# Kernel optimization log

Hardware: AMD Instinct MI355X
Metric: run time of the kernel (lower is better)

Reference implementation:

```python
import jax, jax.numpy as jnp
import numpy as np

U = 8          # units per modular layer
B = 16384      # batch
IN = 512       # input feature dim
H = 512        # modular hidden dim
NC = 62        # n_class


def _aggregate(P, h):
    # P: [T, F] policy link matrix; h: [F, B, D] per-unit features.
    # agg[t] = sum_f P[t,f] * h[f], normalized by row-sum when row-sum > 0.
    s = jnp.einsum('tf,fbd->tbd', P, h)
    row = P.sum(axis=1)                      # [T]
    safe = jnp.where(row > 0, row, 1.0)[:, None, None]
    return jnp.where((row > 0)[:, None, None], s / safe, s)


def setup_inputs() -> dict:
    key = jax.random.key(0)
    ks = jax.random.split(key, 12)
    s_in = 1.0 / np.sqrt(IN)
    s_h = 1.0 / np.sqrt(H)
    return {
        'x': jax.random.normal(ks[0], (B, IN), jnp.float32),
        'policy1': jax.random.uniform(ks[1], (U * U,), jnp.float32),
        'policy2': jax.random.uniform(ks[2], (U * U,), jnp.float32),
        'policy_final': jax.random.uniform(ks[3], (U,), jnp.float32),
        'W0': jax.random.uniform(ks[4], (U, IN, H), jnp.float32, -s_in, s_in),
        'b0': jax.random.uniform(ks[5], (U, H), jnp.float32, -s_in, s_in),
        'W1': jax.random.uniform(ks[6], (U, H, H), jnp.float32, -s_h, s_h),
        'b1': jax.random.uniform(ks[7], (U, H), jnp.float32, -s_h, s_h),
        'W2': jax.random.uniform(ks[8], (U, H, NC), jnp.float32, -s_h, s_h),
        'b2': jax.random.uniform(ks[9], (U, NC), jnp.float32, -s_h, s_h),
    }


def reference(x, policy1, policy2, policy_final, W0, b0, W1, b1, W2, b2):
    # Layer 0 (input modular layer): policy_list[0] is forced to all-ones,
    # so every unit sees x unscaled. Each unit: Linear + ReLU.
    h0 = jax.nn.relu(jnp.einsum('bi,uid->ubd', x, W0) + b0[:, None, :])  # [U,B,H]

    # Mid layer: policy-gated weighted-sum aggregation, then per-unit Linear+ReLU.
    a1 = _aggregate(policy1.reshape(U, U), h0)
    h1 = jax.nn.relu(jnp.einsum('ubi,uid->ubd', a1, W1) + b1[:, None, :])

    # Output modular layer: aggregate then per-unit Linear (no activation).
    a2 = _aggregate(policy2.reshape(U, U), h1)
    h2 = jnp.einsum('ubi,uic->ubc', a2, W2) + b2[:, None, :]  # [U,B,NC]

    # Final gating. Original code divides by divider INSIDE the unit loop
    # (every iteration), so replicate that recurrence exactly.
    d = policy_final.sum()
    inv = jnp.where(d > 0, 1.0 / jnp.where(d > 0, d, 1.0), 1.0)
    out = jnp.zeros((B, NC), jnp.float32)
    for j in range(U):  # fixed small unit count, not a data dim
        out = (out + h2[j] * policy_final[j]) * inv
    return out
```

## Files before the change

kernel.cpp:

```cpp
#include <hip/hip_runtime.h>

#define U_   8
#define B_   16384
#define NC_  62

typedef __attribute__((ext_vector_type(8))) short bfrag;
typedef __attribute__((ext_vector_type(4))) float facc;

__device__ __forceinline__ float bf2f(unsigned int lo16) {
    union { unsigned int i; float f; } v;
    v.i = lo16 << 16;
    return v.f;
}
__device__ __forceinline__ unsigned short f2bf(float f) {
    unsigned int x = __float_as_uint(f);
    return (unsigned short)((x + 0x7fffu + ((x >> 16) & 1u)) >> 16);
}
__device__ __forceinline__ void gl2lds16(const void* g, void* l) {
    __builtin_amdgcn_global_load_lds(
        (const __attribute__((address_space(1))) void*)g,
        (__attribute__((address_space(3))) void*)l, 16, 0, 0);
}
__device__ __forceinline__ void cfence() { asm volatile("" ::: "memory"); }
__device__ __forceinline__ void bar() {
    asm volatile("" ::: "memory");
    __builtin_amdgcn_s_barrier();
    asm volatile("" ::: "memory");
}
#define VMCNT(n) asm volatile("s_waitcnt vmcnt(" #n ")" ::: "memory")

__global__ void prep_kernel(const float* __restrict__ p1, const float* __restrict__ p2,
                            const float* __restrict__ pf, const float* __restrict__ b2,
                            float* __restrict__ P1n, float* __restrict__ P2n,
                            float* __restrict__ wfin, float* __restrict__ cconst)
{
    int t = threadIdx.x;
    if (t >= 64) return;
    int row = t >> 3;
    float s1 = 0.f, s2 = 0.f;
    for (int f = 0; f < 8; f++) { s1 += p1[row * 8 + f]; s2 += p2[row * 8 + f]; }
    P1n[t] = p1[t] * (s1 > 0.f ? 1.f / s1 : 1.f);
    P2n[t] = p2[t] * (s2 > 0.f ? 1.f / s2 : 1.f);
    float d = 0.f;
    for (int j = 0; j < 8; j++) d += pf[j];
    float inv = d > 0.f ? 1.f / d : 1.f;
    float wv[8];
    for (int j = 0; j < 8; j++) {
        float v = pf[j];
        for (int i = j; i < 8; i++) v *= inv;
        wv[j] = v;
    }
    if (t < 8) wfin[t] = wv[t];
    float cc = 0.f;
    if (t < NC_) for (int u = 0; u < 8; u++) cc += wv[u] * b2[u * NC_ + t];
    cconst[t] = cc;
}

__global__ __launch_bounds__(256) void reorder_w0(
    const float* __restrict__ W0, unsigned short* __restrict__ W0r)
{
    __shared__ float tile[32][33];
    const int u  = blockIdx.z;
    const int n0 = blockIdx.x * 32, k0 = blockIdx.y * 32;
    const int tx = threadIdx.x & 31, ty = threadIdx.x >> 5;
    const float* Wb = W0 + (long)u * 512 * 512;
#pragma unroll
    for (int i = 0; i < 4; i++)
        tile[ty + i * 8][tx] = Wb[(long)(k0 + ty + i * 8) * 512 + n0 + tx];
    __syncthreads();
#pragma unroll
    for (int i = 0; i < 4; i++) {
        int n = n0 + ty + i * 8, k = k0 + tx;
        int np = (n >> 5) * 256 + u * 32 + (n & 31);
        W0r[(long)np * 512 + k] = f2bf(tile[tx][ty + i * 8]);
    }
}

__global__ __launch_bounds__(256) void transpose_w(
    const float* __restrict__ W, unsigned short* __restrict__ Wt)
{
    __shared__ float tile[32][33];
    const int u  = blockIdx.z;
    const int n0 = blockIdx.x * 32, k0 = blockIdx.y * 32;
    const int tx = threadIdx.x & 31, ty = threadIdx.x >> 5;
    const float* Wb = W + (long)u * 512 * 512;
#pragma unroll
    for (int i = 0; i < 4; i++)
        tile[ty + i * 8][tx] = Wb[(long)(k0 + ty + i * 8) * 512 + n0 + tx];
    __syncthreads();
    unsigned short* Wo = Wt + (long)u * 512 * 512;
#pragma unroll
    for (int i = 0; i < 4; i++) {
        int n = n0 + ty + i * 8, k = k0 + tx;
        Wo[(long)n * 512 + k] = f2bf(tile[tx][ty + i * 8]);
    }
}

__global__ __launch_bounds__(256) void wout_build(
    const float* __restrict__ W2, const float* __restrict__ P2n,
    const float* __restrict__ wfin, unsigned short* __restrict__ Woutt)
{
    const int c   = threadIdx.x & 63;
    const int row = blockIdx.x * 4 + (threadIdx.x >> 6);
    const int f = row >> 9, k = row & 511;
    float s = 0.f;
    if (c < NC_) {
#pragma unroll
        for (int u = 0; u < 8; u++)
            s += wfin[u] * P2n[u * 8 + f] * W2[((long)u * 512 + k) * NC_ + c];
    }
    Woutt[(long)c * 4096 + row] = f2bf(s);
}

__global__ __launch_bounds__(256) void convert_x(
    const float* __restrict__ x, unsigned short* __restrict__ xb, long n)
{
    long i = ((long)blockIdx.x * 256 + threadIdx.x) * 8;
    if (i >= n) return;
    const float4* xp = (const float4*)(x + i);
    float4 a = xp[0], b = xp[1];
    uint4 o;
    o.x = f2bf(a.x) | ((unsigned)f2bf(a.y) << 16);
    o.y = f2bf(a.z) | ((unsigned)f2bf(a.w) << 16);
    o.z = f2bf(b.x) | ((unsigned)f2bf(b.y) << 16);
    o.w = f2bf(b.z) | ((unsigned)f2bf(b.w) << 16);
    *(uint4*)(xb + i) = o;
}

__global__ __launch_bounds__(512, 2) void gemm0_mix(
    const unsigned short* __restrict__ xb, const unsigned short* __restrict__ W0r,
    const float* __restrict__ b0, const float* __restrict__ P1n,
    unsigned short* __restrict__ a1, long plane)
{
    __shared__ __align__(16) unsigned short sm[49152];
    const int tid = threadIdx.x, w = tid >> 6, lane = tid & 63;
    const int flat = blockIdx.x;
    const int xcd = flat & 7, seq = flat >> 3;
    const int ng = xcd * 2 + (seq & 1);
    const long mBase = (long)(seq >> 1) * 128;

    const int lr = lane >> 3;
    const int lg = (lane & 7) ^ lr;
    const int wm = w >> 2, wn = w & 3;
    const int r = lane & 15, q = lane >> 4;
    const int x7 = r & 7;

    facc acc[4][4];
#pragma unroll
    for (int i = 0; i < 4; i++)
#pragma unroll
        for (int j = 0; j < 4; j++) acc[i][j] = (facc){0.f, 0.f, 0.f, 0.f};

    auto stage = [&](int buf, int kt) {
        const int k0 = kt * 64;
        unsigned short* dA = sm + buf * 8192;
        unsigned short* dB = sm + 16384 + buf * 16384;
#pragma unroll
        for (int i = 0; i < 2; i++) {
            const int c = w + i * 8;
            gl2lds16(xb + (mBase + c * 8 + lr) * 512 + k0 + lg * 8, dA + c * 512);
        }
#pragma unroll
        for (int i = 0; i < 4; i++) {
            const int c = w * 4 + i;
            gl2lds16(W0r + ((long)ng * 256 + c * 8 + lr) * 512 + k0 + lg * 8,
                     dB + c * 512);
        }
    };
    auto compute = [&](int buf) {
        const unsigned short* sA = sm + buf * 8192;
        const unsigned short* sB = sm + 16384 + buf * 16384;
#pragma unroll
        for (int h = 0; h < 2; h++) {
            const int xg = ((h * 4 + q) ^ x7) * 8;
            bfrag aF[4], bF[4];
#pragma unroll
            for (int mt = 0; mt < 4; mt++)
                aF[mt] = *(const bfrag*)&sA[(wm * 64 + mt * 16 + r) * 64 + xg];
#pragma unroll
            for (int nt = 0; nt < 4; nt++)
                bF[nt] = *(const bfrag*)&sB[(wn * 64 + nt * 16 + r) * 64 + xg];
#pragma unroll
            for (int mt = 0; mt < 4; mt++)
#pragma unroll
                for (int nt = 0; nt < 4; nt++)
                    acc[mt][nt] = __builtin_amdgcn_mfma_f32_16x16x32_bf16(
                        aF[mt], bF[nt], acc[mt][nt], 0, 0, 0);
        }
    };

    stage(0, 0);
    cfence();
    stage(1, 1);
    VMCNT(6);
    bar();
#pragma unroll
    for (int t = 0; t < 8; ++t) {
        compute(t & 1);
        if (t <= 5) {
            bar();
            stage(t & 1, t + 2);
            VMCNT(6);
            bar();
        } else if (t == 6) {
            VMCNT(0);
            bar();
        } else {
            bar();
        }
    }

#pragma unroll
    for (int nt = 0; nt < 4; nt++) {
        const int cl = wn * 64 + nt * 16 + r;
        const float bv = b0[(cl >> 5) * 512 + ng * 32 + (cl & 31)];
#pragma unroll
        for (int mt = 0; mt < 4; mt++) {
            const int rowb = wm * 64 + mt * 16 + q * 4;
#pragma unroll
            for (int rg = 0; rg < 4; rg++) {
                float v = acc[mt][nt][rg] + bv;
                v = v > 0.f ? v : 0.f;
                sm[(rowb + rg) * 264 + cl] = f2bf(v);
            }
        }
    }
    __syncthreads();

    float pw[64];
#pragma unroll
    for (int i = 0; i < 64; i++) pw[i] = P1n[i];
    const int row = tid >> 2, fs = (tid & 3) * 8;
    float hv[8][8];
#pragma unroll
    for (int u = 0; u < 8; u++) {
        bfrag hx = *(const bfrag*)&sm[row * 264 + u * 32 + fs];
#pragma unroll
        for (int j = 0; j < 8; j++)
            hv[u][j] = bf2f((unsigned int)(unsigned short)hx[j]);
    }
    const long rowOff = (mBase + row) * 512 + ng * 32 + fs;
#pragma unroll
    for (int t = 0; t < 8; t++) {
        float o[8];
#pragma unroll
        for (int j = 0; j < 8; j++) {
            float s = 0.f;
#pragma unroll
            for (int u = 0; u < 8; u++) s = fmaf(pw[t * 8 + u], hv[u][j], s);
            o[j] = s;
        }
        uint4 ov;
        ov.x = f2bf(o[0]) | ((unsigned)f2bf(o[1]) << 16);
        ov.y = f2bf(o[2]) | ((unsigned)f2bf(o[3]) << 16);
        ov.z = f2bf(o[4]) | ((unsigned)f2bf(o[5]) << 16);
        ov.w = f2bf(o[6]) | ((unsigned)f2bf(o[7]) << 16);
        *(uint4*)(a1 + (long)t * plane + rowOff) = ov;
    }
}

__global__ __launch_bounds__(256, 2) void gemm_h(
    const unsigned short* __restrict__ a1,
    const unsigned short* __restrict__ W1t,
    const float* __restrict__ b1,
    unsigned short* __restrict__ h1, long plane)
{
    __shared__ __align__(16) unsigned short sm[32768];
    const int tid = threadIdx.x, w = tid >> 6, lane = tid & 63;
    const int flat = blockIdx.x;
    const int u = flat & 7, seq = flat >> 3;
    const int nBase = (seq & 3) * 128;
    const long mBase = (long)(seq >> 2) * 128;

    const int lr = lane >> 3, lg = (lane & 7) ^ lr;
    const int wm = w >> 1, wn = w & 1;
    const int r = lane & 15, q = lane >> 4;
    const int x7 = r & 7;

    const unsigned short* Ab = a1 + (long)u * plane;
    const unsigned short* Bb = W1t + ((long)u * 512 + nBase) * 512;

    facc acc[4][4];
#pragma unroll
    for (int i = 0; i < 4; i++)
#pragma unroll
        for (int j = 0; j < 4; j++) acc[i][j] = (facc){0.f, 0.f, 0.f, 0.f};

    auto stage = [&](int buf, int kt) {
        const int k0 = kt * 64;
        unsigned short* dA = sm + buf * 8192;
        unsigned short* dB = sm + 16384 + buf * 8192;
#pragma unroll
        for (int i = 0; i < 4; i++) {
            const int c = w * 4 + i;
            gl2lds16(Ab + (mBase + c * 8 + lr) * 512 + k0 + lg * 8, dA + c * 512);
            gl2lds16(Bb + (long)(c * 8 + lr) * 512 + k0 + lg * 8, dB + c * 512);
        }
    };
    auto compute = [&](int buf) {
        const unsigned short* sA = sm + buf * 8192;
        const unsigned short* sB = sm + 16384 + buf * 8192;
#pragma unroll
        for (int h = 0; h < 2; h++) {
            const int xg = ((h * 4 + q) ^ x7) * 8;
            bfrag aF[4], bF[4];
#pragma unroll
            for (int mt = 0; mt < 4; mt++)
                aF[mt] = *(const bfrag*)&sA[(wm * 64 + mt * 16 + r) * 64 + xg];
#pragma unroll
            for (int nt = 0; nt < 4; nt++)
                bF[nt] = *(const bfrag*)&sB[(wn * 64 + nt * 16 + r) * 64 + xg];
#pragma unroll
            for (int mt = 0; mt < 4; mt++)
#pragma unroll
                for (int nt = 0; nt < 4; nt++)
                    acc[mt][nt] = __builtin_amdgcn_mfma_f32_16x16x32_bf16(
                        aF[mt], bF[nt], acc[mt][nt], 0, 0, 0);
        }
    };

    stage(0, 0);
    cfence();
    stage(1, 1);
    VMCNT(8);
    bar();
#pragma unroll
    for (int t = 0; t < 8; ++t) {
        compute(t & 1);
        if (t <= 5) {
            bar();
            stage(t & 1, t + 2);
            VMCNT(8);
            bar();
        } else if (t == 6) {
            VMCNT(0);
            bar();
        } else {
            bar();
        }
    }

#pragma unroll
    for (int nt = 0; nt < 4; nt++) {
        const int col = wn * 64 + nt * 16 + r;
        const float bv = b1[u * 512 + nBase + col];
#pragma unroll
        for (int mt = 0; mt < 4; mt++) {
            const int rowb = wm * 64 + mt * 16 + q * 4;
#pragma unroll
            for (int rg = 0; rg < 4; rg++) {
                float v = acc[mt][nt][rg] + bv;
                v = v > 0.f ? v : 0.f;
                sm[(rowb + rg) * 136 + col] = f2bf(v);
            }
        }
    }
    __syncthreads();

    unsigned short* Cb = h1 + (long)u * plane + mBase * 512 + nBase;
#pragma unroll
    for (int it = 0; it < 8; it++) {
        const int g = tid + it * 256;
        const int row = g >> 4, gr = g & 15;
        *(uint4*)(Cb + (long)row * 512 + gr * 8) = *(const uint4*)&sm[row * 136 + gr * 8];
    }
}

__global__ __launch_bounds__(256, 1) void gemm_out(
    const unsigned short* __restrict__ h1,
    const unsigned short* __restrict__ Bt,
    float* __restrict__ partial, long plane, int Bc)
{
    __shared__ __align__(16) unsigned short sm[16384];
    const int tid = threadIdx.x, w = tid >> 6, lane = tid & 63;
    const int flat = blockIdx.x;
    const int kc = flat & 1;
    const long mBase = (long)(flat >> 1) * 64;

    const int lr = lane >> 3, lg = (lane & 7) ^ lr;
    const int wm = w >> 1, wn = w & 1;
    const int r = lane & 15, q = lane >> 4;
    const int x7 = r & 7;

    facc acc[2][2];
#pragma unroll
    for (int i = 0; i < 2; i++)
#pragma unroll
        for (int j = 0; j < 2; j++) acc[i][j] = (facc){0.f, 0.f, 0.f, 0.f};

    auto stage = [&](int buf, int it) {
        const int u = kc * 4 + (it >> 3);
        const int kk = (it & 7) * 64;
        unsigned short* dA = sm + buf * 4096;
        unsigned short* dB = sm + 8192 + buf * 4096;
#pragma unroll
        for (int i = 0; i < 2; i++) {
            const int c = w * 2 + i;
            gl2lds16(h1 + (long)u * plane + (mBase + c * 8 + lr) * 512 + kk + lg * 8,
                     dA + c * 512);
            gl2lds16(Bt + (long)(c * 8 + lr) * 4096 + u * 512 + kk + lg * 8,
                     dB + c * 512);
        }
    };
    auto compute = [&](int buf) {
        const unsigned short* sA = sm + buf * 4096;
        const unsigned short* sB = sm + 8192 + buf * 4096;
#pragma unroll
        for (int h = 0; h < 2; h++) {
            const int xg = ((h * 4 + q) ^ x7) * 8;
            bfrag aF[2], bF[2];
#pragma unroll
            for (int mt = 0; mt < 2; mt++)
                aF[mt] = *(const bfrag*)&sA[(wm * 32 + mt * 16 + r) * 64 + xg];
#pragma unroll
            for (int nt = 0; nt < 2; nt++)
                bF[nt] = *(const bfrag*)&sB[(wn * 32 + nt * 16 + r) * 64 + xg];
#pragma unroll
            for (int mt = 0; mt < 2; mt++)
#pragma unroll
                for (int nt = 0; nt < 2; nt++)
                    acc[mt][nt] = __builtin_amdgcn_mfma_f32_16x16x32_bf16(
                        aF[mt], bF[nt], acc[mt][nt], 0, 0, 0);
        }
    };

    stage(0, 0);
    cfence();
    stage(1, 1);
    VMCNT(4);
    bar();
#pragma unroll
    for (int t = 0; t < 32; ++t) {
        compute(t & 1);
        if (t <= 29) {
            bar();
            stage(t & 1, t + 2);
            VMCNT(4);
            bar();
        } else if (t == 30) {
            VMCNT(0);
            bar();
        }
    }

    float* pb = partial + ((long)kc * Bc + mBase) * 64;
#pragma unroll
    for (int nt = 0; nt < 2; nt++) {
        const int col = wn * 32 + nt * 16 + r;
#pragma unroll
        for (int mt = 0; mt < 2; mt++) {
#pragma unroll
            for (int rg = 0; rg < 4; rg++) {
                const int row = wm * 32 + mt * 16 + q * 4 + rg;
                pb[(long)row * 64 + col] = acc[mt][nt][rg];
            }
        }
    }
}

__global__ __launch_bounds__(256) void reduce_out(
    const float* __restrict__ partial, const float* __restrict__ cconst,
    float* __restrict__ out, int Bc)
{
    const long flat = (long)blockIdx.x * 256 + threadIdx.x;
    const long row = flat >> 2;
    const int cg = (int)(flat & 3) * 16;
    float s[16];
#pragma unroll
    for (int j = 0; j < 16; j++) s[j] = 0.f;
#pragma unroll
    for (int kc = 0; kc < 2; kc++) {
        const float4* p = (const float4*)(partial + ((long)kc * Bc + row) * 64 + cg);
#pragma unroll
        for (int v4 = 0; v4 < 4; v4++) {
            float4 v = p[v4];
            s[v4 * 4 + 0] += v.x; s[v4 * 4 + 1] += v.y;
            s[v4 * 4 + 2] += v.z; s[v4 * 4 + 3] += v.w;
        }
    }
#pragma unroll
    for (int j = 0; j < 16; j++) {
        const int c = cg + j;
        if (c < NC_) out[row * NC_ + c] = s[j] + cconst[c];
    }
}

extern "C" void kernel_launch(void* const* d_in, const int* in_sizes, int n_in,
                              void* d_out, int out_size, void* d_ws, size_t ws_size,
                              hipStream_t stream)
{
    const float* x  = (const float*)d_in[0];
    const float* p1 = (const float*)d_in[1];
    const float* p2 = (const float*)d_in[2];
    const float* pf = (const float*)d_in[3];
    const float* W0 = (const float*)d_in[4];
    const float* b0 = (const float*)d_in[5];
    const float* W1 = (const float*)d_in[6];
    const float* b1 = (const float*)d_in[7];
    const float* W2 = (const float*)d_in[8];
    const float* b2 = (const float*)d_in[9];
    float* out = (float*)d_out;

    char* ws = (char*)d_ws;
    size_t off = 0;
    auto alloc = [&](size_t bytes) -> void* {
        void* p = ws + off;
        off += (bytes + 255) & ~(size_t)255;
        return p;
    };
    float* P1n    = (float*)alloc(64 * sizeof(float));
    float* P2n    = (float*)alloc(64 * sizeof(float));
    float* wfin   = (float*)alloc(8 * sizeof(float));
    float* cconst = (float*)alloc(64 * sizeof(float));
    unsigned short* W0r   = (unsigned short*)alloc((size_t)4096 * 512 * 2);
    unsigned short* W1t   = (unsigned short*)alloc((size_t)U_ * 512 * 512 * 2);
    unsigned short* Woutt = (unsigned short*)alloc((size_t)64 * 4096 * 2);
    unsigned short* xb    = (unsigned short*)alloc((size_t)B_ * 512 * 2);

    size_t remain = ws_size > off ? ws_size - off : 0;
    int Bc = 2048;
    for (int cand = B_; cand >= 2048; cand >>= 1) {
        size_t need = 2ull * 8 * cand * 512 * 2 + 2ull * cand * 64 * 4 + 1024;
        if (need <= remain) { Bc = cand; break; }
    }
    unsigned short* a1 = (unsigned short*)alloc(8ull * Bc * 512 * 2);
    unsigned short* h1 = (unsigned short*)alloc(8ull * Bc * 512 * 2);
    float* partial     = (float*)alloc(2ull * Bc * 64 * 4);

    prep_kernel<<<1, 64, 0, stream>>>(p1, p2, pf, b2, P1n, P2n, wfin, cconst);
    reorder_w0<<<dim3(16, 16, 8), 256, 0, stream>>>(W0, W0r);
    transpose_w<<<dim3(16, 16, 8), 256, 0, stream>>>(W1, W1t);
    wout_build<<<dim3(1024), 256, 0, stream>>>(W2, P2n, wfin, Woutt);
    convert_x<<<dim3(B_ * 512 / 8 / 256), 256, 0, stream>>>(x, xb, (long)B_ * 512);

    const int Mb = Bc / 128;
    const long plane = (long)Bc * 512;
    for (int bb = 0; bb < B_; bb += Bc) {
        gemm0_mix<<<dim3(16 * Mb), 512, 0, stream>>>(
            xb + (long)bb * 512, W0r, b0, P1n, a1, plane);
        gemm_h<<<dim3(32 * Mb), 256, 0, stream>>>(a1, W1t, b1, h1, plane);
        gemm_out<<<dim3(2 * (Bc / 64)), 256, 0, stream>>>(h1, Woutt, partial, plane, Bc);
        reduce_out<<<dim3(Bc / 64), 256, 0, stream>>>(
            partial, cconst, out + (long)bb * NC_, Bc);
    }
}
```

Measured before the change: 315.6 us.

## Triple-buffer GEMM pipelines, widen gemm_h tile, add MFMA priority hints

The three GEMM kernels go from double to triple buffering in LDS. The next stage's loads are now issued before the current compute, which removes one barrier per iteration. gemm_h moves to 512-thread blocks with 128x256 tiles to match gemm0_mix and get more reuse of A, and MFMA blocks are wrapped in s_setprio to favour math issue. The cost is more LDS per block (144KB for gemm0/gemm_h at 2 blocks per CU), which may limit occupancy, and fewer blocks for gemm_h.

```diff
diff --git a/kernel.cpp b/kernel.cpp
--- a/kernel.cpp
+++ b/kernel.cpp
@@ -132,7 +132,7 @@
     const float* __restrict__ b0, const float* __restrict__ P1n,
     unsigned short* __restrict__ a1, long plane)
 {
-    __shared__ __align__(16) unsigned short sm[49152];
+    __shared__ __align__(16) unsigned short sm[73728];
     const int tid = threadIdx.x, w = tid >> 6, lane = tid & 63;
     const int flat = blockIdx.x;
     const int xcd = flat & 7, seq = flat >> 3;
@@ -154,7 +154,7 @@
     auto stage = [&](int buf, int kt) {
         const int k0 = kt * 64;
         unsigned short* dA = sm + buf * 8192;
-        unsigned short* dB = sm + 16384 + buf * 16384;
+        unsigned short* dB = sm + 24576 + buf * 16384;
 #pragma unroll
         for (int i = 0; i < 2; i++) {
             const int c = w + i * 8;
@@ -169,7 +169,7 @@
     };
     auto compute = [&](int buf) {
         const unsigned short* sA = sm + buf * 8192;
-        const unsigned short* sB = sm + 16384 + buf * 16384;
+        const unsigned short* sB = sm + 24576 + buf * 16384;
 #pragma unroll
         for (int h = 0; h < 2; h++) {
             const int xg = ((h * 4 + q) ^ x7) * 8;
@@ -180,12 +180,14 @@
 #pragma unroll
             for (int nt = 0; nt < 4; nt++)
                 bF[nt] = *(const bfrag*)&sB[(wn * 64 + nt * 16 + r) * 64 + xg];
+            __builtin_amdgcn_s_setprio(1);
 #pragma unroll
             for (int mt = 0; mt < 4; mt++)
 #pragma unroll
                 for (int nt = 0; nt < 4; nt++)
                     acc[mt][nt] = __builtin_amdgcn_mfma_f32_16x16x32_bf16(
                         aF[mt], bF[nt], acc[mt][nt], 0, 0, 0);
+            __builtin_amdgcn_s_setprio(0);
         }
     };
 
@@ -196,18 +198,11 @@
     bar();
 #pragma unroll
     for (int t = 0; t < 8; ++t) {
-        compute(t & 1);
-        if (t <= 5) {
-            bar();
-            stage(t & 1, t + 2);
-            VMCNT(6);
-            bar();
-        } else if (t == 6) {
-            VMCNT(0);
-            bar();
-        } else {
-            bar();
-        }
+        if (t < 6) stage((t + 2) % 3, t + 2);
+        compute(t % 3);
+        if (t < 6)       { VMCNT(6); bar(); }
+        else if (t == 6) { VMCNT(0); bar(); }
+        else             { bar(); }
     }
 
 #pragma unroll
@@ -259,129 +254,128 @@
     }
 }
 
-__global__ __launch_bounds__(256, 2) void gemm_h(
+__global__ __launch_bounds__(512, 2) void gemm_h(
     const unsigned short* __restrict__ a1,
     const unsigned short* __restrict__ W1t,
     const float* __restrict__ b1,
     unsigned short* __restrict__ h1, long plane)
 {
-    __shared__ __align__(16) unsigned short sm[32768];
+    __shared__ __align__(16) unsigned short sm[73728];
     const int tid = threadIdx.x, w = tid >> 6, lane = tid & 63;
     const int flat = blockIdx.x;
     const int u = flat & 7, seq = flat >> 3;
-    const int nBase = (seq & 3) * 128;
-    const long mBase = (long)(seq >> 2) * 128;
+    const int nBase = (seq & 1) * 256;
+    const long mBase = (long)(seq >> 1) * 128;
+
+    const int lr = lane >> 3, lg = (lane & 7) ^ lr;
+    const int wm = w >> 2, wn = w & 3;
+    const int r = lane & 15, q = lane >> 4;
+    const int x7 = r & 7;
+
+    const unsigned short* Ab = a1 + (long)u * plane;
+    const unsigned short* Bb = W1t + ((long)u * 512 + nBase) * 512;
+
+    facc acc[4][4];
+#pragma unroll
+    for (int i = 0; i < 4; i++)
+#pragma unroll
+        for (int j = 0; j < 4; j++) acc[i][j] = (facc){0.f, 0.f, 0.f, 0.f};
+
+    auto stage = [&](int buf, int kt) {
+        const int k0 = kt * 64;
+        unsigned short* dA = sm + buf * 8192;
+        unsigned short* dB = sm + 24576 + buf * 16384;
+#pragma unroll
+        for (int i = 0; i < 2; i++) {
+            const int c = w + i * 8;
+            gl2lds16(Ab + (mBase + c * 8 + lr) * 512 + k0 + lg * 8, dA + c * 512);
+        }
+#pragma unroll
+        for (int i = 0; i < 4; i++) {
+            const int c = w * 4 + i;
+            gl2lds16(Bb + (long)(c * 8 + lr) * 512 + k0 + lg * 8, dB + c * 512);
+        }
+    };
+    auto compute = [&](int buf) {
+        const unsigned short* sA = sm + buf * 8192;
+        const unsigned short* sB = sm + 24576 + buf * 16384;
+#pragma unroll
+        for (int h = 0; h < 2; h++) {
+            const int xg = ((h * 4 + q) ^ x7) * 8;
+            bfrag aF[4], bF[4];
+#pragma unroll
+            for (int mt = 0; mt < 4; mt++)
+                aF[mt] = *(const bfrag*)&sA[(wm * 64 + mt * 16 + r) * 64 + xg];
+#pragma unroll
+            for (int nt = 0; nt < 4; nt++)
+                bF[nt] = *(const bfrag*)&sB[(wn * 64 + nt * 16 + r) * 64 + xg];
+            __builtin_amdgcn_s_setprio(1);
+#pragma unroll
+            for (int mt = 0; mt < 4; mt++)
+#pragma unroll
+                for (int nt = 0; nt < 4; nt++)
+                    acc[mt][nt] = __builtin_amdgcn_mfma_f32_16x16x32_bf16(
+                        aF[mt], bF[nt], acc[mt][nt], 0, 0, 0);
+            __builtin_amdgcn_s_setprio(0);
+        }
+    };
+
+    stage(0, 0);
+    cfence();
+    stage(1, 1);
+    VMCNT(6);
+    bar();
+#pragma unroll
+    for (int t = 0; t < 8; ++t) {
+        if (t < 6) stage((t + 2) % 3, t + 2);
+        compute(t % 3);
+        if (t < 6)       { VMCNT(6); bar(); }
+        else if (t == 6) { VMCNT(0); bar(); }
+        else             { bar(); }
+    }
+
+#pragma unroll
+    for (int nt = 0; nt < 4; nt++) {
+        const int cl = wn * 64 + nt * 16 + r;
+        const float bv = b1[u * 512 + nBase + cl];
+#pragma unroll
+        for (int mt = 0; mt < 4; mt++) {
+            const int rowb = wm * 64 + mt * 16 + q * 4;
+#pragma unroll
+            for (int rg = 0; rg < 4; rg++) {
+                float v = acc[mt][nt][rg] + bv;
+                v = v > 0.f ? v : 0.f;
+                sm[(rowb + rg) * 264 + cl] = f2bf(v);
+            }
+        }
+    }
+    __syncthreads();
+
+    unsigned short* Cb = h1 + (long)u * plane + mBase * 512 + nBase;
+#pragma unroll
+    for (int it = 0; it < 8; it++) {
+        const int g = tid + it * 512;
+        const int row = g >> 5, gr = g & 31;
+        *(uint4*)(Cb + (long)row * 512 + gr * 8) = *(const uint4*)&sm[row * 264 + gr * 8];
+    }
+}
+
+__global__ __launch_bounds__(256, 1) void gemm_out(
+    const unsigned short* __restrict__ h1,
+    const unsigned short* __restrict__ Bt,
+    float* __restrict__ partial, long plane, int Bc)
+{
+    __shared__ __align__(16) unsigned short sm[24576];
+    const int tid = threadIdx.x, w = tid >> 6, lane = tid & 63;
+    const int flat = blockIdx.x;
+    const int kc = flat & 1;
+    const long mBase = (long)(flat >> 1) * 64;
 
     const int lr = lane >> 3, lg = (lane & 7) ^ lr;
     const int wm = w >> 1, wn = w & 1;
     const int r = lane & 15, q = lane >> 4;
     const int x7 = r & 7;
 
-    const unsigned short* Ab = a1 + (long)u * plane;
-    const unsigned short* Bb = W1t + ((long)u * 512 + nBase) * 512;
-
-    facc acc[4][4];
-#pragma unroll
-    for (int i = 0; i < 4; i++)
-#pragma unroll
-        for (int j = 0; j < 4; j++) acc[i][j] = (facc){0.f, 0.f, 0.f, 0.f};
-
-    auto stage = [&](int buf, int kt) {
-        const int k0 = kt * 64;
-        unsigned short* dA = sm + buf * 8192;
-        unsigned short* dB = sm + 16384 + buf * 8192;
-#pragma unroll
-        for (int i = 0; i < 4; i++) {
-            const int c = w * 4 + i;
-            gl2lds16(Ab + (mBase + c * 8 + lr) * 512 + k0 + lg * 8, dA + c * 512);
-            gl2lds16(Bb + (long)(c * 8 + lr) * 512 + k0 + lg * 8, dB + c * 512);
-        }
-    };
-    auto compute = [&](int buf) {
-        const unsigned short* sA = sm + buf * 8192;
-        const unsigned short* sB = sm + 16384 + buf * 8192;
-#pragma unroll
-        for (int h = 0; h < 2; h++) {
-            const int xg = ((h * 4 + q) ^ x7) * 8;
-            bfrag aF[4], bF[4];
-#pragma unroll
-            for (int mt = 0; mt < 4; mt++)
-                aF[mt] = *(const bfrag*)&sA[(wm * 64 + mt * 16 + r) * 64 + xg];
-#pragma unroll
-            for (int nt = 0; nt < 4; nt++)
-                bF[nt] = *(const bfrag*)&sB[(wn * 64 + nt * 16 + r) * 64 + xg];
-#pragma unroll
-            for (int mt = 0; mt < 4; mt++)
-#pragma unroll
-                for (int nt = 0; nt < 4; nt++)
-                    acc[mt][nt] = __builtin_amdgcn_mfma_f32_16x16x32_bf16(
-                        aF[mt], bF[nt], acc[mt][nt], 0, 0, 0);
-        }
-    };
-
-    stage(0, 0);
-    cfence();
-    stage(1, 1);
-    VMCNT(8);
-    bar();
-#pragma unroll
-    for (int t = 0; t < 8; ++t) {
-        compute(t & 1);
-        if (t <= 5) {
-            bar();
-            stage(t & 1, t + 2);
-            VMCNT(8);
-            bar();
-        } else if (t == 6) {
-            VMCNT(0);
-            bar();
-        } else {
-            bar();
-        }
-    }
-
-#pragma unroll
-    for (int nt = 0; nt < 4; nt++) {
-        const int col = wn * 64 + nt * 16 + r;
-        const float bv = b1[u * 512 + nBase + col];
-#pragma unroll
-        for (int mt = 0; mt < 4; mt++) {
-            const int rowb = wm * 64 + mt * 16 + q * 4;
-#pragma unroll
-            for (int rg = 0; rg < 4; rg++) {
-                float v = acc[mt][nt][rg] + bv;
-                v = v > 0.f ? v : 0.f;
-                sm[(rowb + rg) * 136 + col] = f2bf(v);
-            }
-        }
-    }
-    __syncthreads();
-
-    unsigned short* Cb = h1 + (long)u * plane + mBase * 512 + nBase;
-#pragma unroll
-    for (int it = 0; it < 8; it++) {
-        const int g = tid + it * 256;
-        const int row = g >> 4, gr = g & 15;
-        *(uint4*)(Cb + (long)row * 512 + gr * 8) = *(const uint4*)&sm[row * 136 + gr * 8];
-    }
-}
-
-__global__ __launch_bounds__(256, 1) void gemm_out(
-    const unsigned short* __restrict__ h1,
-    const unsigned short* __restrict__ Bt,
-    float* __restrict__ partial, long plane, int Bc)
-{
-    __shared__ __align__(16) unsigned short sm[16384];
-    const int tid = threadIdx.x, w = tid >> 6, lane = tid & 63;
-    const int flat = blockIdx.x;
-    const int kc = flat & 1;
-    const long mBase = (long)(flat >> 1) * 64;
-
-    const int lr = lane >> 3, lg = (lane & 7) ^ lr;
-    const int wm = w >> 1, wn = w & 1;
-    const int r = lane & 15, q = lane >> 4;
-    const int x7 = r & 7;
-
     facc acc[2][2];
 #pragma unroll
     for (int i = 0; i < 2; i++)
@@ -392,7 +386,7 @@
         const int u = kc * 4 + (it >> 3);
         const int kk = (it & 7) * 64;
         unsigned short* dA = sm + buf * 4096;
-        unsigned short* dB = sm + 8192 + buf * 4096;
+        unsigned short* dB = sm + 12288 + buf * 4096;
 #pragma unroll
         for (int i = 0; i < 2; i++) {
             const int c = w * 2 + i;
@@ -404,7 +398,7 @@
     };
     auto compute = [&](int buf) {
         const unsigned short* sA = sm + buf * 4096;
-        const unsigned short* sB = sm + 8192 + buf * 4096;
+        const unsigned short* sB = sm + 12288 + buf * 4096;
 #pragma unroll
         for (int h = 0; h < 2; h++) {
             const int xg = ((h * 4 + q) ^ x7) * 8;
@@ -415,12 +409,14 @@
 #pragma unroll
             for (int nt = 0; nt < 2; nt++)
                 bF[nt] = *(const bfrag*)&sB[(wn * 32 + nt * 16 + r) * 64 + xg];
+            __builtin_amdgcn_s_setprio(1);
 #pragma unroll
             for (int mt = 0; mt < 2; mt++)
 #pragma unroll
                 for (int nt = 0; nt < 2; nt++)
                     acc[mt][nt] = __builtin_amdgcn_mfma_f32_16x16x32_bf16(
                         aF[mt], bF[nt], acc[mt][nt], 0, 0, 0);
+            __builtin_amdgcn_s_setprio(0);
         }
     };
 
@@ -431,16 +427,10 @@
     bar();
 #pragma unroll
     for (int t = 0; t < 32; ++t) {
-        compute(t & 1);
-        if (t <= 29) {
-            bar();
-            stage(t & 1, t + 2);
-            VMCNT(4);
-            bar();
-        } else if (t == 30) {
-            VMCNT(0);
-            bar();
-        }
+        if (t < 30) stage((t + 2) % 3, t + 2);
+        compute(t % 3);
+        if (t < 30)       { VMCNT(4); bar(); }
+        else if (t == 30) { VMCNT(0); bar(); }
     }
 
     float* pb = partial + ((long)kc * Bc + mBase) * 64;
@@ -538,7 +528,7 @@
     for (int bb = 0; bb < B_; bb += Bc) {
         gemm0_mix<<<dim3(16 * Mb), 512, 0, stream>>>(
             xb + (long)bb * 512, W0r, b0, P1n, a1, plane);
-        gemm_h<<<dim3(32 * Mb), 256, 0, stream>>>(a1, W1t, b1, h1, plane);
+        gemm_h<<<dim3(16 * Mb), 512, 0, stream>>>(a1, W1t, b1, h1, plane);
         gemm_out<<<dim3(2 * (Bc / 64)), 256, 0, stream>>>(h1, Woutt, partial, plane, Bc);
         reduce_out<<<dim3(Bc / 64), 256, 0, stream>>>(
             partial, cconst, out + (long)bb * NC_, Bc);
```

Measured after the change: 338.4 us. 7.2% more time.

## Retile GEMMs to 128x256 per 4-wave block with BK=32 and LDS-wait barriers

Applied to the files above, without the earlier changes.

gemm0_mix moves from 512 threads with 4x4 tiles per wave to 256 threads with 4x8 tiles per wave. gemm_h widens its block N tile from 128 to 256, which halves its grid. Both kernels shrink the K step from 64 to 32 with a new XOR swizzle and double the iteration count. Barriers after compute now wait on lgkmcnt(0) before reusing the buffer. The larger per-wave tiles raise MFMA work per LDS fragment load and cut the shared-memory footprint, at the cost of higher accumulator register pressure and more barrier round-trips per K.

```diff
diff --git a/kernel.cpp b/kernel.cpp
--- a/kernel.cpp
+++ b/kernel.cpp
@@ -24,6 +24,11 @@
 __device__ __forceinline__ void cfence() { asm volatile("" ::: "memory"); }
 __device__ __forceinline__ void bar() {
     asm volatile("" ::: "memory");
+    __builtin_amdgcn_s_barrier();
+    asm volatile("" ::: "memory");
+}
+__device__ __forceinline__ void barL() {
+    asm volatile("s_waitcnt lgkmcnt(0)" ::: "memory");
     __builtin_amdgcn_s_barrier();
     asm volatile("" ::: "memory");
 }
@@ -127,66 +132,62 @@
     *(uint4*)(xb + i) = o;
 }
 
-__global__ __launch_bounds__(512, 2) void gemm0_mix(
+__global__ __launch_bounds__(256, 2) void gemm0_mix(
     const unsigned short* __restrict__ xb, const unsigned short* __restrict__ W0r,
     const float* __restrict__ b0, const float* __restrict__ P1n,
     unsigned short* __restrict__ a1, long plane)
 {
-    __shared__ __align__(16) unsigned short sm[49152];
+    __shared__ __align__(16) unsigned short sm[33792];
     const int tid = threadIdx.x, w = tid >> 6, lane = tid & 63;
     const int flat = blockIdx.x;
     const int xcd = flat & 7, seq = flat >> 3;
     const int ng = xcd * 2 + (seq & 1);
     const long mBase = (long)(seq >> 1) * 128;
 
-    const int lr = lane >> 3;
-    const int lg = (lane & 7) ^ lr;
-    const int wm = w >> 2, wn = w & 3;
+    const int lr = lane >> 2;
+    const int lg = (lane & 3) ^ ((lane >> 3) & 3);
+    const int wm = w >> 1, wn = w & 1;
     const int r = lane & 15, q = lane >> 4;
-    const int x7 = r & 7;
-
-    facc acc[4][4];
+    const int xq = (q ^ ((r >> 1) & 3)) * 8;
+
+    facc acc[4][8];
 #pragma unroll
     for (int i = 0; i < 4; i++)
 #pragma unroll
-        for (int j = 0; j < 4; j++) acc[i][j] = (facc){0.f, 0.f, 0.f, 0.f};
+        for (int j = 0; j < 8; j++) acc[i][j] = (facc){0.f, 0.f, 0.f, 0.f};
 
     auto stage = [&](int buf, int kt) {
-        const int k0 = kt * 64;
-        unsigned short* dA = sm + buf * 8192;
-        unsigned short* dB = sm + 16384 + buf * 16384;
+        const int k0 = kt * 32;
+        unsigned short* dA = sm + buf * 4096;
+        unsigned short* dB = sm + 8192 + buf * 8192;
 #pragma unroll
         for (int i = 0; i < 2; i++) {
-            const int c = w + i * 8;
-            gl2lds16(xb + (mBase + c * 8 + lr) * 512 + k0 + lg * 8, dA + c * 512);
+            const int c = w * 2 + i;
+            gl2lds16(xb + (mBase + c * 16 + lr) * 512 + k0 + lg * 8, dA + c * 512);
         }
 #pragma unroll
         for (int i = 0; i < 4; i++) {
             const int c = w * 4 + i;
-            gl2lds16(W0r + ((long)ng * 256 + c * 8 + lr) * 512 + k0 + lg * 8,
+            gl2lds16(W0r + ((long)ng * 256 + c * 16 + lr) * 512 + k0 + lg * 8,
                      dB + c * 512);
         }
     };
     auto compute = [&](int buf) {
-        const unsigned short* sA = sm + buf * 8192;
-        const unsigned short* sB = sm + 16384 + buf * 16384;
-#pragma unroll
-        for (int h = 0; h < 2; h++) {
-            const int xg = ((h * 4 + q) ^ x7) * 8;
-            bfrag aF[4], bF[4];
-#pragma unroll
-            for (int mt = 0; mt < 4; mt++)
-                aF[mt] = *(const bfrag*)&sA[(wm * 64 + mt * 16 + r) * 64 + xg];
-#pragma unroll
-            for (int nt = 0; nt < 4; nt++)
-                bF[nt] = *(const bfrag*)&sB[(wn * 64 + nt * 16 + r) * 64 + xg];
-#pragma unroll
-            for (int mt = 0; mt < 4; mt++)
-#pragma unroll
-                for (int nt = 0; nt < 4; nt++)
-                    acc[mt][nt] = __builtin_amdgcn_mfma_f32_16x16x32_bf16(
-                        aF[mt], bF[nt], acc[mt][nt], 0, 0, 0);
-        }
+        const unsigned short* sA = sm + buf * 4096;
+        const unsigned short* sB = sm + 8192 + buf * 8192;
+        bfrag aF[4], bF[8];
+#pragma unroll
+        for (int mt = 0; mt < 4; mt++)
+            aF[mt] = *(const bfrag*)&sA[(wm * 64 + mt * 16 + r) * 32 + xq];
+#pragma unroll
+        for (int nt = 0; nt < 8; nt++)
+            bF[nt] = *(const bfrag*)&sB[(wn * 128 + nt * 16 + r) * 32 + xq];
+#pragma unroll
+        for (int mt = 0; mt < 4; mt++)
+#pragma unroll
+            for (int nt = 0; nt < 8; nt++)
+                acc[mt][nt] = __builtin_amdgcn_mfma_f32_16x16x32_bf16(
+                    aF[mt], bF[nt], acc[mt][nt], 0, 0, 0);
     };
 
     stage(0, 0);
@@ -195,24 +196,24 @@
     VMCNT(6);
     bar();
 #pragma unroll
-    for (int t = 0; t < 8; ++t) {
+    for (int t = 0; t < 16; ++t) {
         compute(t & 1);
-        if (t <= 5) {
-            bar();
+        if (t <= 13) {
+            barL();
             stage(t & 1, t + 2);
             VMCNT(6);
             bar();
-        } else if (t == 6) {
+        } else if (t == 14) {
             VMCNT(0);
             bar();
         } else {
-            bar();
-        }
-    }
-
-#pragma unroll
-    for (int nt = 0; nt < 4; nt++) {
-        const int cl = wn * 64 + nt * 16 + r;
+            barL();
+        }
+    }
+
+#pragma unroll
+    for (int nt = 0; nt < 8; nt++) {
+        const int cl = wn * 128 + nt * 16 + r;
         const float bv = b0[(cl >> 5) * 512 + ng * 32 + (cl & 31)];
 #pragma unroll
         for (int mt = 0; mt < 4; mt++) {
@@ -230,32 +231,40 @@
     float pw[64];
 #pragma unroll
     for (int i = 0; i < 64; i++) pw[i] = P1n[i];
-    const int row = tid >> 2, fs = (tid & 3) * 8;
-    float hv[8][8];
+    const int row = tid >> 1, fs0 = (tid & 1) * 16;
+    float hv[8][16];
 #pragma unroll
     for (int u = 0; u < 8; u++) {
-        bfrag hx = *(const bfrag*)&sm[row * 264 + u * 32 + fs];
-#pragma unroll
-        for (int j = 0; j < 8; j++)
-            hv[u][j] = bf2f((unsigned int)(unsigned short)hx[j]);
-    }
-    const long rowOff = (mBase + row) * 512 + ng * 32 + fs;
+        bfrag ha = *(const bfrag*)&sm[row * 264 + u * 32 + fs0];
+        bfrag hb = *(const bfrag*)&sm[row * 264 + u * 32 + fs0 + 8];
+#pragma unroll
+        for (int j = 0; j < 8; j++) {
+            hv[u][j]     = bf2f((unsigned int)(unsigned short)ha[j]);
+            hv[u][j + 8] = bf2f((unsigned int)(unsigned short)hb[j]);
+        }
+    }
+    const long rowOff = (mBase + row) * 512 + ng * 32 + fs0;
 #pragma unroll
     for (int t = 0; t < 8; t++) {
-        float o[8];
-#pragma unroll
-        for (int j = 0; j < 8; j++) {
+        float o[16];
+#pragma unroll
+        for (int j = 0; j < 16; j++) {
             float s = 0.f;
 #pragma unroll
             for (int u = 0; u < 8; u++) s = fmaf(pw[t * 8 + u], hv[u][j], s);
             o[j] = s;
         }
-        uint4 ov;
-        ov.x = f2bf(o[0]) | ((unsigned)f2bf(o[1]) << 16);
-        ov.y = f2bf(o[2]) | ((unsigned)f2bf(o[3]) << 16);
-        ov.z = f2bf(o[4]) | ((unsigned)f2bf(o[5]) << 16);
-        ov.w = f2bf(o[6]) | ((unsigned)f2bf(o[7]) << 16);
-        *(uint4*)(a1 + (long)t * plane + rowOff) = ov;
+        uint4 ov0, ov1;
+        ov0.x = f2bf(o[0])  | ((unsigned)f2bf(o[1])  << 16);
+        ov0.y = f2bf(o[2])  | ((unsigned)f2bf(o[3])  << 16);
+        ov0.z = f2bf(o[4])  | ((unsigned)f2bf(o[5])  << 16);
+        ov0.w = f2bf(o[6])  | ((unsigned)f2bf(o[7])  << 16);
+        ov1.x = f2bf(o[8])  | ((unsigned)f2bf(o[9])  << 16);
+        ov1.y = f2bf(o[10]) | ((unsigned)f2bf(o[11]) << 16);
+        ov1.z = f2bf(o[12]) | ((unsigned)f2bf(o[13]) << 16);
+        ov1.w = f2bf(o[14]) | ((unsigned)f2bf(o[15]) << 16);
+        *(uint4*)(a1 + (long)t * plane + rowOff)     = ov0;
+        *(uint4*)(a1 + (long)t * plane + rowOff + 8) = ov1;
     }
 }
 
@@ -265,85 +274,86 @@
     const float* __restrict__ b1,
     unsigned short* __restrict__ h1, long plane)
 {
-    __shared__ __align__(16) unsigned short sm[32768];
+    __shared__ __align__(16) unsigned short sm[33792];
     const int tid = threadIdx.x, w = tid >> 6, lane = tid & 63;
     const int flat = blockIdx.x;
     const int u = flat & 7, seq = flat >> 3;
-    const int nBase = (seq & 3) * 128;
-    const long mBase = (long)(seq >> 2) * 128;
-
-    const int lr = lane >> 3, lg = (lane & 7) ^ lr;
+    const int nBase = (seq & 1) * 256;
+    const long mBase = (long)(seq >> 1) * 128;
+
+    const int lr = lane >> 2;
+    const int lg = (lane & 3) ^ ((lane >> 3) & 3);
     const int wm = w >> 1, wn = w & 1;
     const int r = lane & 15, q = lane >> 4;
-    const int x7 = r & 7;
+    const int xq = (q ^ ((r >> 1) & 3)) * 8;
 
     const unsigned short* Ab = a1 + (long)u * plane;
     const unsigned short* Bb = W1t + ((long)u * 512 + nBase) * 512;
 
-    facc acc[4][4];
+    facc acc[4][8];
 #pragma unroll
     for (int i = 0; i < 4; i++)
 #pragma unroll
-        for (int j = 0; j < 4; j++) acc[i][j] = (facc){0.f, 0.f, 0.f, 0.f};
+        for (int j = 0; j < 8; j++) acc[i][j] = (facc){0.f, 0.f, 0.f, 0.f};
 
     auto stage = [&](int buf, int kt) {
-        const int k0 = kt * 64;
-        unsigned short* dA = sm + buf * 8192;
-        unsigned short* dB = sm + 16384 + buf * 8192;
+        const int k0 = kt * 32;
+        unsigned short* dA = sm + buf * 4096;
+        unsigned short* dB = sm + 8192 + buf * 8192;
+#pragma unroll
+        for (int i = 0; i < 2; i++) {
+            const int c = w * 2 + i;
+            gl2lds16(Ab + (mBase + c * 16 + lr) * 512 + k0 + lg * 8, dA + c * 512);
+        }
 #pragma unroll
         for (int i = 0; i < 4; i++) {
             const int c = w * 4 + i;
-            gl2lds16(Ab + (mBase + c * 8 + lr) * 512 + k0 + lg * 8, dA + c * 512);
-            gl2lds16(Bb + (long)(c * 8 + lr) * 512 + k0 + lg * 8, dB + c * 512);
+            gl2lds16(Bb + (long)(c * 16 + lr) * 512 + k0 + lg * 8, dB + c * 512);
         }
     };
     auto compute = [&](int buf) {
-        const unsigned short* sA = sm + buf * 8192;
-        const unsigned short* sB = sm + 16384 + buf * 8192;
-#pragma unroll
-        for (int h = 0; h < 2; h++) {
-            const int xg = ((h * 4 + q) ^ x7) * 8;
-            bfrag aF[4], bF[4];
-#pragma unroll
-            for (int mt = 0; mt < 4; mt++)
-                aF[mt] = *(const bfrag*)&sA[(wm * 64 + mt * 16 + r) * 64 + xg];
-#pragma unroll
-            for (int nt = 0; nt < 4; nt++)
-                bF[nt] = *(const bfrag*)&sB[(wn * 64 + nt * 16 + r) * 64 + xg];
-#pragma unroll
-            for (int mt = 0; mt < 4; mt++)
-#pragma unroll
-                for (int nt = 0; nt < 4; nt++)
-                    acc[mt][nt] = __builtin_amdgcn_mfma_f32_16x16x32_bf16(
-                        aF[mt], bF[nt], acc[mt][nt], 0, 0, 0);
-        }
+        const unsigned short* sA = sm + buf * 4096;
+        const unsigned short* sB = sm + 8192 + buf * 8192;
+        bfrag aF[4], bF[8];
+#pragma unroll
+        for (int mt = 0; mt < 4; mt++)
+            aF[mt] = *(const bfrag*)&sA[(wm * 64 + mt * 16 + r) * 32 + xq];
+#pragma unroll
+        for (int nt = 0; nt < 8; nt++)
+            bF[nt] = *(const bfrag*)&sB[(wn * 128 + nt * 16 + r) * 32 + xq];
+#pragma unroll
+        for (int mt = 0; mt < 4; mt++)
+#pragma unroll
+            for (int nt = 0; nt < 8; nt++)
+                acc[mt][nt] = __builtin_amdgcn_mfma_f32_16x16x32_bf16(
+                    aF[mt], bF[nt], acc[mt][nt], 0, 0, 0);
     };
 
     stage(0, 0);
     cfence();
     stage(1, 1);
-    VMCNT(8);
+    VMCNT(6);
     bar();
 #pragma unroll
-    for (int t = 0; t < 8; ++t) {
+    for (int t = 0; t < 16; ++t) {
         compute(t & 1);
-        if (t <= 5) {
+        if (t <= 13) {
+            barL();
+            stage(t & 1, t + 2);
+            VMCNT(6);
             bar();
-            stage(t & 1, t + 2);
-            VMCNT(8);
-            bar();
-        } else if (t == 6) {
+        } else if (t == 14) {
             VMCNT(0);
             bar();
         } else {
-            bar();
-        }
-    }
-
-#pragma unroll
-    for (int nt = 0; nt < 4; nt++) {
-        const int col = wn * 64 + nt * 16 + r;
-        const float bv = b1[u * 512 + nBase + col];
+            barL();
+        }
+    }
+
+#pragma unroll
+    for (int nt = 0; nt < 8; nt++) {
+        const int cl = wn * 128 + nt * 16 + r;
+        const float bv = b1[u * 512 + nBase + cl];
 #pragma unroll
         for (int mt = 0; mt < 4; mt++) {
             const int rowb = wm * 64 + mt * 16 + q * 4;
@@ -351,7 +361,7 @@
             for (int rg = 0; rg < 4; rg++) {
                 float v = acc[mt][nt][rg] + bv;
                 v = v > 0.f ? v : 0.f;
-                sm[(rowb + rg) * 136 + col] = f2bf(v);
+                sm[(rowb + rg) * 264 + cl] = f2bf(v);
             }
         }
     }
@@ -359,10 +369,10 @@
 
     unsigned short* Cb = h1 + (long)u * plane + mBase * 512 + nBase;
 #pragma unroll
-    for (int it = 0; it < 8; it++) {
+    for (int it = 0; it < 16; it++) {
         const int g = tid + it * 256;
-        const int row = g >> 4, gr = g & 15;
-        *(uint4*)(Cb + (long)row * 512 + gr * 8) = *(const uint4*)&sm[row * 136 + gr * 8];
+        const int row = g >> 5, gr = g & 31;
+        *(uint4*)(Cb + (long)row * 512 + gr * 8) = *(const uint4*)&sm[row * 264 + gr * 8];
     }
 }
 
@@ -433,7 +443,7 @@
     for (int t = 0; t < 32; ++t) {
         compute(t & 1);
         if (t <= 29) {
-            bar();
+            barL();
             stage(t & 1, t + 2);
             VMCNT(4);
             bar();
@@ -536,9 +546,9 @@
     const int Mb = Bc / 128;
     const long plane = (long)Bc * 512;
     for (int bb = 0; bb < B_; bb += Bc) {
-        gemm0_mix<<<dim3(16 * Mb), 512, 0, stream>>>(
+        gemm0_mix<<<dim3(16 * Mb), 256, 0, stream>>>(
             xb + (long)bb * 512, W0r, b0, P1n, a1, plane);
-        gemm_h<<<dim3(32 * Mb), 256, 0, stream>>>(a1, W1t, b1, h1, plane);
+        gemm_h<<<dim3(16 * Mb), 256, 0, stream>>>(a1, W1t, b1, h1, plane);
         gemm_out<<<dim3(2 * (Bc / 64)), 256, 0, stream>>>(h1, Woutt, partial, plane, Bc);
         reduce_out<<<dim3(Bc / 64), 256, 0, stream>>>(
             partial, cconst, out + (long)bb * NC_, Bc);
```

Measured after the change: 342.4 us. +8.5%, slower.
